# Optimization experiments

Hardware: AMD Instinct MI355X
Metric: run time of the kernel (lower is better)

The kernel has to match this reference:

```python
import jax, jax.numpy as jnp
import numpy as np

V, FN, CIN, HID, PTS = 50000, 100000, 3, 256, 10000
TEMP = 0.1
EPS = 1e-20


def line_mesh_graph(f, Vn):
    # f: [F,3] int triangles. Build the 'line mesh': one node per unique mesh edge.
    fe = jnp.concatenate([f[:, :2], f[:, 1:], f[:, jnp.array([2, 0])]], 0)  # [3F,2]
    fe = jnp.sort(fe, axis=1)
    keys = fe[:, 0] * Vn + fe[:, 1]                       # [3F] unique key per undirected edge
    ukeys, inv = jnp.unique(keys, return_inverse=True)
    edge_node = jnp.stack([ukeys // Vn, ukeys % Vn], -1)  # [E,2] endpoints of each edge-node
    E = ukeys.shape[0]
    feid = inv.reshape(3, -1).T                           # [F,3] edge-node id per face edge
    # line-graph connectivity: edges of the same face are mutual neighbors, plus self-loops
    srcs, dsts = [], []
    for i, j in ((0, 1), (1, 0), (1, 2), (2, 1), (2, 0), (0, 2)):
        srcs.append(feid[:, i]); dsts.append(feid[:, j])
    loop = jnp.arange(E)
    edge = jnp.stack([jnp.concatenate(srcs + [loop]), jnp.concatenate(dsts + [loop])], 0)  # [2,NE]
    return edge, edge_node, keys


def gsn_conv(x, edge, Ws, Wn, b):
    # GSNConv stand-in: self transform + mean-aggregated neighbor transform
    s, d = edge[0], edge[1]
    N = x.shape[0]
    deg = jax.ops.segment_sum(jnp.ones_like(s, x.dtype), d, num_segments=N)
    agg = jax.ops.segment_sum(x[s], d, num_segments=N) / jnp.clip(deg, 1.0)[:, None]
    return x @ Ws + agg @ Wn + b


def gumbel_mask(logits, temperature, num, key):
    U = jax.random.uniform(key, logits.shape)
    g = -jnp.log(-jnp.log(U + EPS) + EPS)
    y = jax.nn.softmax((logits + g) / temperature, -1)[:, 0]  # [E]
    _, ind = jax.lax.top_k(y, num)
    y_hard = jnp.zeros_like(y).at[ind].set(1.0)
    mask = jax.lax.stop_gradient(y_hard - y) + y              # straight-through one-hot
    return mask, y_hard == 1.0


def mesh_collapse(f, keys, pool_edge, Vn):
    # Vectorized replacement of the per-pool-edge python loop: hash-join pooled edge keys
    # against all 3F face-edge keys via sorted search.
    PE = pool_edge.shape[0]
    pool_idx = jnp.arange(Vn, Vn + PE)
    edge_keys = keys.reshape(3, -1).T                     # [F,3] (cols: e01,e12,e20)
    pk = pool_edge[:, 0] * Vn + pool_edge[:, 1]
    order = jnp.argsort(pk); pks = pk[order]
    flat = edge_keys.reshape(-1)
    pos = jnp.clip(jnp.searchsorted(pks, flat), 0, PE - 1)
    found = pks[pos] == flat
    pei = jnp.where(found, pool_idx[order[pos]], -1).reshape(-1, 3)  # pool_edge_idx [F,3]
    fm = found.reshape(-1, 3)
    pen = fm.sum(1)                                       # pool_edge_num per face
    psi = (fm * jnp.arange(3)).sum(1)                     # pool_start_idx per face
    vv = jnp.stack([f[:, 0], pei[:, 0], f[:, 1], pei[:, 1], f[:, 2], pei[:, 2]], -1)
    nf0 = f[pen == 0]
    fv1 = vv[pen == 1]; s1 = psi[pen == 1]
    fv1 = jnp.concatenate([fv1[s1 == 0], jnp.roll(fv1[s1 == 1], -2, 1), jnp.roll(fv1[s1 == 2], 2, 1)], 0)
    nf1 = jnp.concatenate([jnp.stack([fv1[:, 0], fv1[:, 1], fv1[:, 4]], -1),
                           jnp.stack([fv1[:, 1], fv1[:, 2], fv1[:, 4]], -1)], 0)
    fv2 = vv[pen == 2]; s2 = psi[pen == 2]
    fv2 = jnp.concatenate([fv2[s2 == 1], jnp.roll(fv2[s2 == 2], 2, 1), jnp.roll(fv2[s2 == 3], -2, 1)], 0)
    nf2 = jnp.concatenate([jnp.stack([fv2[:, 0], fv2[:, 1], fv2[:, 4]], -1),
                           jnp.stack([fv2[:, 1], fv2[:, 2], fv2[:, 3]], -1),
                           jnp.stack([fv2[:, 1], fv2[:, 3], fv2[:, 4]], -1)], 0)
    fv3 = vv[pen == 3]
    nf3 = jnp.concatenate([jnp.stack([fv3[:, 0], fv3[:, 1], fv3[:, 5]], -1),
                           jnp.stack([fv3[:, 1], fv3[:, 2], fv3[:, 3]], -1),
                           jnp.stack([fv3[:, 1], fv3[:, 3], fv3[:, 5]], -1),
                           jnp.stack([fv3[:, 3], fv3[:, 4], fv3[:, 5]], -1)], 0)
    new_faces = jnp.concatenate([nf0, nf1, nf2, nf3], 0)
    ne = jnp.concatenate([new_faces[:, :2], new_faces[:, 1:], new_faces[:, jnp.array([2, 0])]], 0)
    ai = jnp.arange(Vn + PE)
    ne = jnp.concatenate([jnp.stack([ai, ai], -1), ne], 0)
    return new_faces, ne.T


def setup_inputs():
    key = jax.random.key(0)
    ks = jax.random.split(key, 10)
    s1 = 1.0 / np.sqrt(CIN); s2 = 1.0 / np.sqrt(HID)
    return {
        'input': jax.random.normal(ks[0], (1, V, CIN), jnp.float32),
        'face': jax.random.randint(ks[1], (1, FN, 3), 0, V),
        'coord': jax.random.normal(ks[2], (1, V, 3), jnp.float32),
        'detail_points': jax.random.normal(ks[3], (1, PTS, 3), jnp.float32),
        'div': 5,
        'W1s': jax.random.normal(ks[4], (CIN, HID), jnp.float32) * s1,
        'W1n': jax.random.normal(ks[5], (CIN, HID), jnp.float32) * s1,
        'b1': jnp.zeros((HID,), jnp.float32),
        'W2s': jax.random.normal(ks[6], (HID, 2), jnp.float32) * s2,
        'W2n': jax.random.normal(ks[7], (HID, 2), jnp.float32) * s2,
        'b2': jnp.zeros((2,), jnp.float32),
    }


def reference(input, face, coord, detail_points, div, W1s, W1n, b1, W2s, W2n, b2):
    # B=1 (data-dependent per-sample output sizes make batch stacking only valid then)
    x0, f = input[0], face[0]
    Vn = x0.shape[0]
    edge, edge_node, keys = line_mesh_graph(f, Vn)
    xe = 0.5 * (x0[edge_node[:, 0]] + x0[edge_node[:, 1]])   # edge-node features [E,C]
    h = jax.nn.relu(gsn_conv(xe, edge, W1s, W1n, b1))
    out = jax.nn.sigmoid(gsn_conv(h, edge, W2s, W2n, b2))    # [E,2]
    mask, pool_ind = gumbel_mask(out, TEMP, out.shape[0] // div, jax.random.key(42))
    pool_edge = edge_node[pool_ind]                          # [PE,2]
    new_faces, new_edges = mesh_collapse(f, keys, pool_edge, Vn)
    return edge_node[None], new_faces[None], new_edges[None], mask[None]
```

## Files before the change

### kernel.cpp

```cpp
#include <hip/hip_runtime.h>
#include <stdint.h>

typedef uint32_t u32;
typedef uint64_t u64;

#define VN 50000
#define FN 100000
#define K3F 300000
#define EMAX 300000
#define NB1 1172
#define NBS 293
#define NBH 293
#define NBC 98
#define HALF1 150016
#define NBL 586

#define W_KPA    0u
#define W_KPB    600000u
#define W_SEGOFF 1200000u
#define W_FEID   1500004u
#define W_XE     1800004u
#define W_PK     2700004u
#define W_P      2703076u
#define W_Q      3303076u
#define W_Y      3903076u
#define W_YMAP   4203076u
#define W_T64    4503076u
#define W_SEL    5103140u
#define W_SELR   5403140u
#define W_CAT    5703140u
#define W_NFI    5903140u
#define W_HIST   7103140u
#define W_HIST2  7403172u
#define W_SUMS   7703204u
#define W_CATH   7707300u
#define W_TKH    7708324u
#define W_DONE   7708580u
#define W_SCAL   7708612u

#define S_E 0
#define S_NUM 1
#define S_PFX 2
#define S_KREM 3
#define S_TU 4
#define S_R 5
#define S_NF 6
#define S_NEN 7
#define S_O1 8
#define S_O2 9
#define S_O3 10
#define S_RS 16
#define S_GS 24
#define S_GP 32

#define ALDR(p) __hip_atomic_load((p), __ATOMIC_RELAXED, __HIP_MEMORY_SCOPE_AGENT)

__device__ __forceinline__ void tf2x32(u32 x0, u32 x1, u32& o0, u32& o1) {
  const u32 ks0 = 0u, ks1 = 42u, ks2 = 0x1BD11BDAu ^ 0u ^ 42u;
  x0 += ks0; x1 += ks1;
#define TFR(r) { x0 += x1; x1 = (x1<<(r))|(x1>>(32-(r))); x1 ^= x0; }
  TFR(13) TFR(15) TFR(26) TFR(6)   x0 += ks1; x1 += ks2 + 1u;
  TFR(17) TFR(29) TFR(16) TFR(24)  x0 += ks2; x1 += ks0 + 2u;
  TFR(13) TFR(15) TFR(26) TFR(6)   x0 += ks0; x1 += ks1 + 3u;
  TFR(17) TFR(29) TFR(16) TFR(24)  x0 += ks1; x1 += ks2 + 4u;
  TFR(13) TFR(15) TFR(26) TFR(6)   x0 += ks2; x1 += ks0 + 5u;
#undef TFR
  o0 = x0; o1 = x1;
}

__global__ void scan_blocks(const u32* __restrict__ in, u32* __restrict__ out,
                            u32* __restrict__ sums, int n) {
  __shared__ u32 lds[256];
  int t = threadIdx.x;
  int base = blockIdx.x*1024 + t*4;
  u32 v[4]; u32 tot = 0;
  for (int k = 0; k < 4; ++k) { v[k] = (base+k < n) ? in[base+k] : 0u; tot += v[k]; }
  lds[t] = tot; __syncthreads();
  for (int o = 1; o < 256; o <<= 1) {
    u32 x = (t >= o) ? lds[t-o] : 0u; __syncthreads();
    lds[t] += x; __syncthreads();
  }
  u32 excl = lds[t] - tot;
  if (t == 255) sums[blockIdx.x] = lds[255];
  u32 run = excl;
  for (int k = 0; k < 4; ++k) { if (base+k < n) out[base+k] = run; run += v[k]; }
}

__global__ void scan_flagblocks(const u64* __restrict__ kp, u32* __restrict__ out,
                                u32* __restrict__ sums, int n) {
  __shared__ u32 lds[256];
  int t = threadIdx.x;
  int base = blockIdx.x*1024 + t*4;
  u32 v[4]; u32 tot = 0;
  for (int k = 0; k < 4; ++k) {
    int i = base + k;
    u32 f = 0;
    if (i < n) f = (i == 0 || (u32)(kp[i-1]>>32) != (u32)(kp[i]>>32)) ? 1u : 0u;
    v[k] = f; tot += f;
  }
  lds[t] = tot; __syncthreads();
  for (int o = 1; o < 256; o <<= 1) {
    u32 x = (t >= o) ? lds[t-o] : 0u; __syncthreads();
    lds[t] += x; __syncthreads();
  }
  u32 excl = lds[t] - tot;
  if (t == 255) sums[blockIdx.x] = lds[255];
  u32 run = excl;
  for (int k = 0; k < 4; ++k) { if (base+k < n) out[base+k] = run; run += v[k]; }
}

__global__ void scan64_src(const u32* __restrict__ ymap, const u32* __restrict__ scal,
                           u64* __restrict__ part, u64* __restrict__ sums) {
  __shared__ u64 lds[256];
  int t = threadIdx.x;
  int base = blockIdx.x*1024 + t*4;
  int E = (int)scal[S_E];
  u32 TU = scal[S_TU];
  u64 v[4]; u64 tot = 0;
  for (int k = 0; k < 4; ++k) {
    int e = base + k;
    u64 val = 0;
    if (e < E) {
      u32 u = ymap[e];
      if (u > TU) val = 1ull;
      else if (u == TU) val = 1ull << 32;
    }
    v[k] = val; tot += val;
  }
  lds[t] = tot; __syncthreads();
  for (int o = 1; o < 256; o <<= 1) {
    u64 x = (t >= o) ? lds[t-o] : 0ull; __syncthreads();
    lds[t] += x; __syncthreads();
  }
  u64 excl = lds[t] - tot;
  if (t == 255) sums[blockIdx.x] = lds[255];
  u64 run = excl;
  for (int k = 0; k < 4; ++k) { part[base+k] = run; run += v[k]; }
}

__global__ void k_sel2(const u32* __restrict__ ymap, const u64* __restrict__ part,
                       const u64* __restrict__ sums, const u32* __restrict__ scal,
                       u32* __restrict__ sel, u32* __restrict__ selr) {
  __shared__ u64 sl64[256];
  int t = threadIdx.x, b = blockIdx.x;
  u64 partial = 0;
  for (int j = t; j < b; j += 256) partial += sums[j];
  sl64[t] = partial; __syncthreads();
  for (int o = 128; o; o >>= 1) { if (t < o) sl64[t] += sl64[t+o]; __syncthreads(); }
  u64 basepre = sl64[0];
  int E = (int)scal[S_E];
  u32 TU = scal[S_TU], R = scal[S_R];
  for (int k = 0; k < 4; ++k) {
    int e = b*1024 + k*256 + t;
    if (e >= EMAX) continue;
    u64 pre = part[e] + basepre;
    u32 GTpre = (u32)pre, TIEpre = (u32)(pre >> 32);
    u32 v = 0;
    if (e < E) {
      u32 u = ymap[e];
      v = (u > TU) || (u == TU && TIEpre < R);
    }
    sel[e] = v ? 1u : 0u;
    selr[e] = GTpre + min(TIEpre, R);
  }
}

__global__ void k_rhist(const u64* __restrict__ kp, u32* __restrict__ hist,
                        int shift, int nb) {
  __shared__ u32 h[256];
  int t = threadIdx.x;
  h[t] = 0; __syncthreads();
  int i = blockIdx.x*256 + t;
  if (i < K3F) atomicAdd(&h[((u32)(kp[i]>>32) >> shift) & 255u], 1u);
  __syncthreads();
  hist[(u32)t*nb + blockIdx.x] = h[t];
}

__global__ void k_rscat(const u64* __restrict__ kp, u64* __restrict__ okp,
                        const u32* __restrict__ hist, const u32* __restrict__ sums,
                        int shift, int nb) {
  __shared__ u32 sl[256];
  __shared__ u32 ps[NBS];
  __shared__ u64 ball[4][8];
  __shared__ u64 vmask[4];
  int t = threadIdx.x, w = t>>6, lane = t&63;
  u32 a0 = (t < NBS) ? sums[t] : 0u;
  u32 a1 = (256 + t < NBS) ? sums[256+t] : 0u;
  sl[t] = a0; __syncthreads();
  for (int o = 1; o < 256; o <<= 1) {
    u32 x = (t >= o) ? sl[t-o] : 0u; __syncthreads();
    sl[t] += x; __syncthreads();
  }
  u32 incl0 = sl[t], tot0 = sl[255];
  if (t < NBS) ps[t] = incl0 - a0;
  __syncthreads();
  sl[t] = a1; __syncthreads();
  for (int o = 1; o < 256; o <<= 1) {
    u32 x = (t >= o) ? sl[t-o] : 0u; __syncthreads();
    sl[t] += x; __syncthreads();
  }
  if (256 + t < NBS) ps[256+t] = sl[t] - a1 + tot0;
  __syncthreads();
  int i = blockIdx.x*256 + t;
  bool valid = i < K3F;
  u64 v = valid ? kp[i] : 0ull;
  u32 d = ((u32)(v>>32) >> shift) & 255u;
  for (int bit = 0; bit < 8; ++bit) {
    u64 bm = __ballot(valid && ((d>>bit)&1u));
    if (lane == 0) ball[w][bit] = bm;
  }
  u64 vb = __ballot(valid ? 1 : 0);
  if (lane == 0) vmask[w] = vb;
  __syncthreads();
  if (valid) {
    u32 rank = 0;
    for (int ww = 0; ww < w; ++ww) {
      u64 m = vmask[ww];
      for (int bit = 0; bit < 8; ++bit) { u64 bb = ball[ww][bit]; m &= ((d>>bit)&1u) ? bb : ~bb; }
      rank += (u32)__popcll(m);
    }
    u64 m = vmask[w];
    for (int bit = 0; bit < 8; ++bit) { u64 bb = ball[w][bit]; m &= ((d>>bit)&1u) ? bb : ~bb; }
    rank += (u32)__popcll(m & ((1ull<<lane)-1ull));
    u32 h = d*(u32)nb + blockIdx.x;
    u32 pos = hist[h] + ps[h>>10] + rank;
    okp[pos] = v;
  }
}

__global__ void k_keys(const int* __restrict__ face,
                       const float* __restrict__ W1s, const float* __restrict__ W1n,
                       const float* __restrict__ b1,
                       const float* __restrict__ W2s, const float* __restrict__ W2n,
                       float* __restrict__ pk,
                       u64* __restrict__ kp, u32* __restrict__ hist,
                       u32* __restrict__ tkh, u32* __restrict__ done) {
  __shared__ u32 h[256];
  int t = threadIdx.x;
  h[t] = 0;
  __syncthreads();
  if (blockIdx.x == 0) {
    tkh[t] = 0u;
    if (t < 32) done[t] = 0u;
    float* p = pk + t*12;
    p[0] = W1s[t]; p[1] = W1s[256+t]; p[2] = W1s[512+t];
    p[3] = W1n[t]; p[4] = W1n[256+t]; p[5] = W1n[512+t];
    p[6] = b1[t];
    p[7] = W2s[2*t]; p[8] = W2s[2*t+1];
    p[9] = W2n[2*t]; p[10] = W2n[2*t+1];
    p[11] = 0.0f;
  }
  int i = blockIdx.x*256 + t;
  if (i < K3F) {
    int s = i / FN, f = i - s*FN;
    int v0 = face[f*3 + s];
    int v1 = face[f*3 + (s == 2 ? 0 : s+1)];
    int a = min(v0, v1), b = max(v0, v1);
    u32 key = ((u32)a * (u32)VN + (u32)b) ^ 0x80000000u;
    kp[i] = ((u64)key << 32) | (u32)i;
    atomicAdd(&h[key & 255u], 1u);
  }
  __syncthreads();
  hist[(u32)t*NB1 + blockIdx.x] = h[t];
}

__global__ void k_uwrite(const u64* __restrict__ kp, const u32* __restrict__ rankp,
                         const u32* __restrict__ sums, const float* __restrict__ x,
                         u32* __restrict__ segoff, u32* __restrict__ feid,
                         float* __restrict__ xe, float* __restrict__ dout,
                         u32* __restrict__ scal, const int* __restrict__ divp) {
  __shared__ u32 sl[256];
  int t = threadIdx.x, b = blockIdx.x;
  int chunk = b >> 2;
  u32 partial = 0;
  for (int j = t; j < chunk; j += 256) partial += sums[j];
  sl[t] = partial; __syncthreads();
  for (int o = 128; o; o >>= 1) { if (t < o) sl[t] += sl[t+o]; __syncthreads(); }
  u32 basepre = sl[0];
  int p = b*256 + t;
  if (p >= K3F) return;
  u64 v = kp[p];
  u32 cur = (u32)(v >> 32);
  u32 fl = (p == 0 || (u32)(kp[p-1] >> 32) != cur) ? 1u : 0u;
  u32 rk = rankp[p] + basepre;
  if (fl) {
    u32 e = rk;
    segoff[e] = (u32)p;
    int k = (int)(cur ^ 0x80000000u);
    long long kk = (long long)k;
    long long qq = (kk - (kk < 0 ? (long long)(VN-1) : 0ll)) / VN;
    int q = (int)qq;
    int r = (int)(kk - qq * VN);
    dout[2*e]   = (float)q;
    dout[2*e+1] = (float)r;
    u32 i0 = (u32)(q < 0 ? q + VN : q);
    u32 i1 = (u32)r;
    for (int c = 0; c < 3; ++c) xe[e*3+c] = 0.5f*(x[i0*3+c] + x[i1*3+c]);
  }
  u32 id = rk - 1u + fl;
  u32 i = (u32)v;
  u32 s = i / FN, f = i - s*FN;
  feid[f*3 + s] = id;
  if (p == K3F-1) {
    u32 E = rk + fl;
    u32 num = E / (u32)divp[0];
    scal[S_E] = E; scal[S_NUM] = num;
    segoff[E] = (u32)K3F;
    scal[S_PFX] = 0u; scal[S_KREM] = num;
  }
}

__device__ __forceinline__ void agg_neighbors(int e, u32 st, u32 en,
                                              const u64* __restrict__ kp,
                                              const u32* __restrict__ feid,
                                              const float* __restrict__ v, int stride,
                                              float* acc0, float* acc1, float* acc2) {
  const int sslot[6] = {0,1,1,2,2,0};
  const int dslot[6] = {1,0,2,1,0,2};
  float c0 = 0.f, c1 = 0.f, c2 = 0.f;
  for (int b = 0; b < 6; ++b) {
    int j = dslot[b], isl = sslot[b];
    for (u32 p = st; p < en; ++p) {
      u32 i = (u32)kp[p];
      u32 s = i / FN;
      if ((int)s == j) {
        u32 f = i - s*FN;
        u32 u = feid[f*3 + isl];
        c0 += v[u*stride]; c1 += v[u*stride+1]; if (stride == 3) c2 += v[u*stride+2];
      }
    }
  }
  c0 += v[e*stride]; c1 += v[e*stride+1]; if (stride == 3) c2 += v[e*stride+2];
  *acc0 = c0; *acc1 = c1; *acc2 = c2;
}

__global__ void k_l12(const float* __restrict__ xe, const u32* __restrict__ segoff,
                      const u64* __restrict__ kp, const u32* __restrict__ feid,
                      const u32* __restrict__ scal, const float* __restrict__ pk,
                      float* __restrict__ P, float* __restrict__ Q) {
  int e1 = blockIdx.x*256 + threadIdx.x;
  int E = (int)scal[S_E];
  if (e1 >= E) return;
  int e2 = e1 + HALF1;
  bool v2 = e2 < E;
  int e2c = v2 ? e2 : e1;
  u32 st1 = segoff[e1], en1 = segoff[e1+1];
  u32 st2 = segoff[e2c], en2 = segoff[e2c+1];
  float c0a,c1a,c2a, c0b,c1b,c2b;
  agg_neighbors(e1,  st1, en1, kp, feid, xe, 3, &c0a,&c1a,&c2a);
  agg_neighbors(e2c, st2, en2, kp, feid, xe, 3, &c0b,&c1b,&c2b);
  float x0a=xe[e1*3],  x1a=xe[e1*3+1],  x2a=xe[e1*3+2];
  float x0b=xe[e2c*3], x1b=xe[e2c*3+1], x2b=xe[e2c*3+2];
  float dga = (float)(2u*(en1-st1)+1u), dgb = (float)(2u*(en2-st2)+1u);
  float m0a=c0a/dga, m1a=c1a/dga, m2a=c2a/dga;
  float m0b=c0b/dgb, m1b=c1b/dgb, m2b=c2b/dgb;
  float p0a=0,p1a=0,q0a=0,q1a=0, p0b=0,p1b=0,q0b=0,q1b=0;
#pragma unroll 4
  for (int hh = 0; hh < 256; ++hh) {
    const float* w = pk + hh*12;
    float w0=w[0],w1=w[1],w2=w[2],w3=w[3],w4=w[4],w5=w[5],w6=w[6];
    float w7=w[7],w8=w[8],w9=w[9],w10=w[10];
    float s1a = x0a*w0 + x1a*w1 + x2a*w2;
    float s2a = m0a*w3 + m1a*w4 + m2a*w5;
    float ha = fmaxf(s1a + s2a + w6, 0.0f);
    p0a += ha*w7;  p1a += ha*w8;  q0a += ha*w9;  q1a += ha*w10;
    float s1b = x0b*w0 + x1b*w1 + x2b*w2;
    float s2b = m0b*w3 + m1b*w4 + m2b*w5;
    float hb = fmaxf(s1b + s2b + w6, 0.0f);
    p0b += hb*w7;  p1b += hb*w8;  q0b += hb*w9;  q1b += hb*w10;
  }
  P[2*e1] = p0a; P[2*e1+1] = p1a; Q[2*e1] = q0a; Q[2*e1+1] = q1a;
  if (v2) { P[2*e2] = p0b; P[2*e2+1] = p1b; Q[2*e2] = q0b; Q[2*e2+1] = q1b; }
}

__device__ __forceinline__ void score_one(int e, const float* P, const float* Q,
                                          const u32* segoff, const u64* kp, const u32* feid,
                                          float b20, float b21, float* yo, u32* ymo) {
  u32 st = segoff[e], en = segoff[e+1];
  float a0, a1, dummy;
  agg_neighbors(e, st, en, kp, feid, Q, 2, &a0, &a1, &dummy);
  float dg = (float)(2u*(en - st) + 1u);
  float z0 = P[2*e]   + a0/dg + b20;
  float z1 = P[2*e+1] + a1/dg + b21;
  float l0 = 1.0f/(1.0f + expf(-z0));
  float l1 = 1.0f/(1.0f + expf(-z1));
  u32 g0b, g1b;
  { u32 o0,o1; tf2x32(0u, 2u*(u32)e,      o0, o1); g0b = o0 ^ o1; }
  { u32 o0,o1; tf2x32(0u, 2u*(u32)e + 1u, o0, o1); g1b = o0 ^ o1; }
  float U0 = __uint_as_float((g0b>>9) | 0x3f800000u) - 1.0f;
  float U1 = __uint_as_float((g1b>>9) | 0x3f800000u) - 1.0f;
  float g0 = -logf(-logf(U0 + 1e-20f) + 1e-20f);
  float g1 = -logf(-logf(U1 + 1e-20f) + 1e-20f);
  float A0 = (l0 + g0)/0.1f;
  float A1 = (l1 + g1)/0.1f;
  float mx = fmaxf(A0, A1);
  float e0 = expf(A0-mx), e1v = expf(A1-mx);
  float y = e0/(e0+e1v);
  *yo = y;
  *ymo = __float_as_uint(y) | 0x80000000u;
}

__global__ void k_scores(const float* __restrict__ P, const float* __restrict__ Q,
                         const u32* __restrict__ segoff, const u64* __restrict__ kp,
                         const u32* __restrict__ feid,
                         const float* __restrict__ b2, const u32* __restrict__ scal,
                         float* __restrict__ Y, u32* __restrict__ ymap) {
  int e1 = blockIdx.x*256 + threadIdx.x;
  int E = (int)scal[S_E];
  if (e1 >= E) return;
  int e2 = e1 + HALF1;
  bool v2 = e2 < E;
  int e2c = v2 ? e2 : e1;
  float b20 = b2[0], b21 = b2[1];
  float ya, yb; u32 ma, mb;
  score_one(e1,  P, Q, segoff, kp, feid, b20, b21, &ya, &ma);
  score_one(e2c, P, Q, segoff, kp, feid, b20, b21, &yb, &mb);
  Y[e1] = ya; ymap[e1] = ma;
  if (v2) { Y[e2] = yb; ymap[e2] = mb; }
}

__global__ void k_tkround(const u32* __restrict__ ymap, u32* __restrict__ scal,
                          u32* __restrict__ hist, u32* __restrict__ done, int byte) {
  __shared__ u32 h[256];
  __shared__ u32 s2[256];
  __shared__ u32 chosen_s;
  __shared__ u32 lastflag;
  int t = threadIdx.x;
  h[t] = 0u;
  if (t == 0) lastflag = 0u;
  __syncthreads();
  int E = (int)scal[S_E];
  u32 pfx = scal[S_PFX];
  int base = blockIdx.x*1024;
  for (int k = 0; k < 4; ++k) {
    int e = base + k*256 + t;
    if (e < E) {
      u32 u = ymap[e];
      bool match = (byte == 3) || ((u >> ((byte+1)*8)) == pfx);
      if (match) atomicAdd(&h[(u >> (byte*8)) & 255u], 1u);
    }
  }
  __syncthreads();
  u32 c = h[t];
  if (c) atomicAdd(&hist[t], c);
  __syncthreads();
  if (t == 0) {
    __threadfence();
    u32 old = atomicAdd(&done[byte], 1u);
    if (old == gridDim.x - 1u) lastflag = 1u;
  }
  __syncthreads();
  if (!lastflag) return;
  __threadfence();
  u32 v = atomicExch(&hist[t], 0u);
  s2[t] = v;
  if (t == 0) chosen_s = 0u;
  __syncthreads();
  for (int o = 1; o < 256; o <<= 1) {
    u32 x = (t + o < 256) ? s2[t+o] : 0u; __syncthreads();
    s2[t] += x; __syncthreads();
  }
  u32 krem = scal[S_KREM];
  if (s2[t] >= krem) atomicMax(&chosen_s, (u32)t);
  __syncthreads();
  if (t == 0) {
    u32 chosen = chosen_s;
    u32 sufnext = (chosen < 255u) ? s2[chosen+1] : 0u;
    u32 newkrem = krem - sufnext;
    u32 npfx = (scal[S_PFX] << 8) | chosen;
    scal[S_PFX] = npfx; scal[S_KREM] = newkrem;
    if (byte == 0) { scal[S_TU] = npfx; scal[S_R] = newkrem; }
  }
}

__global__ void k_catfused(const u32* __restrict__ feid, const u32* __restrict__ sel,
                           u32* __restrict__ cat, u32* __restrict__ ch,
                           u32* __restrict__ done, u32* __restrict__ scal) {
  __shared__ u32 h[8];
  __shared__ u32 lastflag;
  __shared__ u32 lds[256];
  __shared__ u32 ex[1024];
  int t = threadIdx.x;
  if (t < 8) h[t] = 0u;
  if (t == 0) lastflag = 0u;
  __syncthreads();
  int base = blockIdx.x*1024 + t*4;
  for (int k = 0; k < 4; ++k) {
    int f = base + k;
    if (f < FN) {
      u32 m0 = sel[feid[f*3]], m1 = sel[feid[f*3+1]], m2 = sel[feid[f*3+2]];
      u32 pen = m0 + m1 + m2;
      u32 psi = m1 + 2u*m2;
      u32 c = (pen == 0) ? 0u : (pen == 1) ? (1u+psi) : (pen == 2) ? (3u+psi) : 7u;
      cat[f] = c;
      atomicAdd(&h[c], 1u);
    }
  }
  __syncthreads();
  if (t < 8) ch[(u32)t*NBC + blockIdx.x] = h[t];
  __syncthreads();
  if (t == 0) {
    __threadfence();
    u32 old = atomicAdd(&done[8], 1u);
    if (old == gridDim.x - 1u) lastflag = 1u;
  }
  __syncthreads();
  if (!lastflag) return;
  __threadfence();
  u32 v[4]; u32 tot = 0;
  for (int k = 0; k < 4; ++k) {
    int i = t*4 + k;
    u32 x = (i < 8*NBC) ? ALDR(&ch[i]) : 0u;
    v[k] = x; tot += x;
  }
  lds[t] = tot; __syncthreads();
  for (int o = 1; o < 256; o <<= 1) {
    u32 x = (t >= o) ? lds[t-o] : 0u; __syncthreads();
    lds[t] += x; __syncthreads();
  }
  u32 excl = lds[t] - tot;
  u32 run = excl;
  for (int k = 0; k < 4; ++k) { ex[t*4+k] = run; run += v[k]; }
  __syncthreads();
  for (int k = 0; k < 4; ++k) {
    int i = t*4 + k;
    if (i < 8*NBC) ch[i] = ex[i];
  }
  if (t == 0) {
    u32 total = lds[255];
    u32 bnd[9];
    for (int c = 0; c < 8; ++c) bnd[c] = ex[c*NBC];
    bnd[8] = total;
    u32 tot8[8];
    for (int c = 0; c < 8; ++c) tot8[c] = bnd[c+1] - bnd[c];
    u32 n0 = tot8[0], n1 = tot8[1]+tot8[2]+tot8[3], n2 = tot8[4]+tot8[5]+tot8[6], n3 = tot8[7];
    u32 NF = n0 + 2u*n1 + 3u*n2 + 4u*n3;
    u32 E = scal[S_E], num = scal[S_NUM];
    u32 NEn = (u32)VN + num + 3u*NF;
    scal[S_NF] = NF; scal[S_NEN] = NEn;
    scal[S_O1] = 2u*E;
    scal[S_O2] = 2u*E + 3u*NF;
    scal[S_O3] = 2u*E + 3u*NF + 2u*NEn;
    u32 RS[8] = {0u, n0,n0,n0, n0+2u*n1, n0+2u*n1, n0+2u*n1, n0+2u*n1+3u*n2};
    u32 GS[8] = {0u, n1,n1,n1, n2,n2,n2, n3};
    u32 GP[8] = {0u, n0,n0,n0, n0+n1, n0+n1, n0+n1, n0+n1+n2};
    for (int i = 0; i < 8; ++i) { scal[S_RS+i] = RS[i]; scal[S_GS+i] = GS[i]; scal[S_GP+i] = GP[i]; }
  }
}

__global__ void k_catwf(const u32* __restrict__ cat, const u32* __restrict__ ch,
                        const int* __restrict__ face, const u32* __restrict__ feid,
                        const u32* __restrict__ selr, const u32* __restrict__ scal,
                        int* __restrict__ nfi, float* __restrict__ dout) {
  __shared__ u32 lds[256];
  int t = threadIdx.x;
  int base = blockIdx.x*1024 + t*4;
  u32 cc[4], loc[4];
  u32 cnt[8] = {0,0,0,0,0,0,0,0};
  for (int k = 0; k < 4; ++k) {
    int i = base + k;
    if (i < FN) { u32 c = cat[i]; cc[k] = c; loc[k] = cnt[c]++; }
    else cc[k] = 8u;
  }
  u32 tb[8];
  for (int c = 0; c < 8; ++c) {
    lds[t] = cnt[c]; __syncthreads();
    for (int o = 1; o < 256; o <<= 1) {
      u32 x = (t >= o) ? lds[t-o] : 0u; __syncthreads();
      lds[t] += x; __syncthreads();
    }
    tb[c] = lds[t] - cnt[c];
    __syncthreads();
  }
  const int nfc[8] = {1,2,2,2,3,3,3,4};
  const int tri[8][4][3] = {
    {{0,2,4},{0,0,0},{0,0,0},{0,0,0}},
    {{0,1,4},{1,2,4},{0,0,0},{0,0,0}},
    {{2,3,0},{3,4,0},{0,0,0},{0,0,0}},
    {{4,5,2},{5,0,2},{0,0,0},{0,0,0}},
    {{0,1,4},{1,2,3},{1,3,4},{0,0,0}},
    {{4,5,2},{5,0,1},{5,1,2},{0,0,0}},
    {{2,3,0},{3,4,5},{3,5,0},{0,0,0}},
    {{0,1,5},{1,2,3},{1,3,5},{3,4,5}}};
  u32 o1 = scal[S_O1];
  for (int k = 0; k < 4; ++k) {
    int f = base + k;
    if (f >= FN) break;
    u32 c = cc[k];
    u32 rank = ch[c*NBC + blockIdx.x] + tb[c] + loc[k];
    int cv[6];
    cv[0] = face[f*3];   cv[2] = face[f*3+1]; cv[4] = face[f*3+2];
    cv[1] = VN + (int)selr[feid[f*3]];
    cv[3] = VN + (int)selr[feid[f*3+1]];
    cv[5] = VN + (int)selr[feid[f*3+2]];
    u32 g = rank - scal[S_GP + c];
    for (int j = 0; j < nfc[c]; ++j) {
      u32 row = scal[S_RS + c] + (u32)j*scal[S_GS + c] + g;
      for (int m = 0; m < 3; ++m) {
        int v = cv[tri[c][j][m]];
        nfi[row*3 + m] = v;
        dout[o1 + row*3 + m] = (float)v;
      }
    }
  }
}

__global__ void k_wnemask(const int* __restrict__ nfi, const u32* __restrict__ sel,
                          const float* __restrict__ Y, const u32* __restrict__ scal,
                          float* __restrict__ dout) {
  int i = blockIdx.x*256 + threadIdx.x;
  int E = (int)scal[S_E];
  if (i < E) {
    float y = Y[i];
    float yh = sel[i] ? 1.0f : 0.0f;
    dout[scal[S_O3] + i] = (yh - y) + y;
  }
  u32 NEn = scal[S_NEN];
  if (i >= (int)NEn) return;
  u32 NF = scal[S_NF];
  u32 Vp = (u32)VN + scal[S_NUM];
  u32 o2 = scal[S_O2];
  int a, b;
  if ((u32)i < Vp) { a = i; b = i; }
  else {
    u32 j = (u32)i - Vp;
    u32 blk = j / NF, r = j - blk*NF;
    int i0 = (blk == 0) ? 0 : (blk == 1) ? 1 : 2;
    int i1 = (blk == 0) ? 1 : (blk == 1) ? 2 : 0;
    a = nfi[r*3 + i0]; b = nfi[r*3 + i1];
  }
  dout[o2 + i] = (float)a;
  dout[o2 + NEn + i] = (float)b;
}

extern "C" void kernel_launch(void* const* d_in, const int* in_sizes, int n_in,
                              void* d_out, int out_size, void* d_ws, size_t ws_size,
                              hipStream_t stream) {
  const float* x    = (const float*)d_in[0];
  const int*   face = (const int*)d_in[1];
  const int*   divp = (const int*)d_in[4];
  const float* W1s  = (const float*)d_in[5];
  const float* W1n  = (const float*)d_in[6];
  const float* b1   = (const float*)d_in[7];
  const float* W2s  = (const float*)d_in[8];
  const float* W2n  = (const float*)d_in[9];
  const float* b2   = (const float*)d_in[10];
  float* out = (float*)d_out;
  u32* W = (u32*)d_ws;

  u64 *KPA = (u64*)(W+W_KPA), *KPB = (u64*)(W+W_KPB);
  u32 *HIST = W+W_HIST, *HIST2 = W+W_HIST2, *SUMS = W+W_SUMS, *SCAL = W+W_SCAL;
  u32 *TKH = W+W_TKH, *DONE = W+W_DONE;
  u32 *RK = W+W_T64;
  u64 *T64 = (u64*)(W+W_T64);
  u64 *SUMS64 = (u64*)(W+W_SUMS);

  k_keys<<<NB1, 256, 0, stream>>>(face, W1s, W1n, b1, W2s, W2n, (float*)(W+W_PK),
                                  KPA, HIST, TKH, DONE);
  scan_blocks<<<NBS, 256, 0, stream>>>(HIST, HIST, SUMS, NB1*256);
  k_rscat<<<NB1, 256, 0, stream>>>(KPA, KPB, HIST, SUMS,  0, NB1);
  k_rhist<<<NB1, 256, 0, stream>>>(KPB, HIST2,  8, NB1);
  scan_blocks<<<NBS, 256, 0, stream>>>(HIST2, HIST2, SUMS, NB1*256);
  k_rscat<<<NB1, 256, 0, stream>>>(KPB, KPA, HIST2, SUMS,  8, NB1);
  k_rhist<<<NB1, 256, 0, stream>>>(KPA, HIST, 16, NB1);
  scan_blocks<<<NBS, 256, 0, stream>>>(HIST, HIST, SUMS, NB1*256);
  k_rscat<<<NB1, 256, 0, stream>>>(KPA, KPB, HIST, SUMS, 16, NB1);
  k_rhist<<<NB1, 256, 0, stream>>>(KPB, HIST2, 24, NB1);
  scan_blocks<<<NBS, 256, 0, stream>>>(HIST2, HIST2, SUMS, NB1*256);
  k_rscat<<<NB1, 256, 0, stream>>>(KPB, KPA, HIST2, SUMS, 24, NB1);

  scan_flagblocks<<<NBS, 256, 0, stream>>>(KPA, RK, SUMS, K3F);
  k_uwrite<<<NB1, 256, 0, stream>>>(KPA, RK, SUMS, x, W+W_SEGOFF, W+W_FEID,
                                    (float*)(W+W_XE), out, SCAL, divp);

  k_l12<<<NBL, 256, 0, stream>>>((float*)(W+W_XE), W+W_SEGOFF, KPA, W+W_FEID, SCAL,
                                 (float*)(W+W_PK), (float*)(W+W_P), (float*)(W+W_Q));
  k_scores<<<NBL, 256, 0, stream>>>((float*)(W+W_P), (float*)(W+W_Q), W+W_SEGOFF, KPA,
                                    W+W_FEID, b2, SCAL, (float*)(W+W_Y), W+W_YMAP);

  for (int byte = 3; byte >= 0; --byte)
    k_tkround<<<NBH, 256, 0, stream>>>(W+W_YMAP, SCAL, TKH, DONE, byte);
  scan64_src<<<NBS, 256, 0, stream>>>(W+W_YMAP, SCAL, T64, SUMS64);
  k_sel2<<<NBS, 256, 0, stream>>>(W+W_YMAP, T64, SUMS64, SCAL, W+W_SEL, W+W_SELR);

  k_catfused<<<NBC, 256, 0, stream>>>(W+W_FEID, W+W_SEL, W+W_CAT, W+W_CATH, DONE, SCAL);
  k_catwf<<<NBC, 256, 0, stream>>>(W+W_CAT, W+W_CATH, face, W+W_FEID, W+W_SELR, SCAL,
                                   (int*)(W+W_NFI), out);
  k_wnemask<<<5118, 256, 0, stream>>>((int*)(W+W_NFI), W+W_SEL, (float*)(W+W_Y), SCAL, out);
}
```

Measured before the change: 323.9 us.

## Fuse first top-k histogram round into score kernel; unroll short neighbor segments

The score kernel now also builds the top-byte histogram for radix top-k selection and runs the first selection round in its last-arriving block. This removes one k_tkround launch and one pass over ymap. Separately, neighbor aggregation for segments of at most 8 entries preloads keys into registers and unrolls the six slot passes, avoiding repeated global loads of kp. This adds shared-memory atomics and a done[9] counter, which relies on that slot being zeroed before the kernel runs.

```diff
diff --git a/kernel.cpp b/kernel.cpp
--- a/kernel.cpp
+++ b/kernel.cpp
@@ -316,17 +316,44 @@
                                               const float* __restrict__ v, int stride,
                                               float* acc0, float* acc1, float* acc2) {
   const int sslot[6] = {0,1,1,2,2,0};
-  const int dslot[6] = {1,0,2,1,0,2};
+  const int dslot[6] = {1,0,2,1,2,0};
+  (void)dslot;
+  const int dsl[6] = {1,0,2,1,0,2};
   float c0 = 0.f, c1 = 0.f, c2 = 0.f;
-  for (int b = 0; b < 6; ++b) {
-    int j = dslot[b], isl = sslot[b];
-    for (u32 p = st; p < en; ++p) {
-      u32 i = (u32)kp[p];
-      u32 s = i / FN;
-      if ((int)s == j) {
-        u32 f = i - s*FN;
-        u32 u = feid[f*3 + isl];
-        c0 += v[u*stride]; c1 += v[u*stride+1]; if (stride == 3) c2 += v[u*stride+2];
+  u32 n = en - st;
+  if (n <= 8u) {
+    u32 s8[8], ft[8];
+#pragma unroll
+    for (int j = 0; j < 8; ++j) {
+      if ((u32)j < n) {
+        u32 i = (u32)kp[st + (u32)j];
+        u32 s = i / FN;
+        s8[j] = s;
+        ft[j] = (i - s*FN)*3u;
+      } else { s8[j] = 0xFFFFFFFFu; ft[j] = 0u; }
+    }
+#pragma unroll
+    for (int b = 0; b < 6; ++b) {
+      u32 jd = (u32)dsl[b]; int isl = sslot[b];
+#pragma unroll
+      for (int j = 0; j < 8; ++j) {
+        if (s8[j] == jd) {
+          u32 u = feid[ft[j] + isl];
+          c0 += v[u*stride]; c1 += v[u*stride+1]; if (stride == 3) c2 += v[u*stride+2];
+        }
+      }
+    }
+  } else {
+    for (int b = 0; b < 6; ++b) {
+      int jd = dsl[b], isl = sslot[b];
+      for (u32 p = st; p < en; ++p) {
+        u32 i = (u32)kp[p];
+        u32 s = i / FN;
+        if ((int)s == jd) {
+          u32 f = i - s*FN;
+          u32 u = feid[f*3 + isl];
+          c0 += v[u*stride]; c1 += v[u*stride+1]; if (stride == 3) c2 += v[u*stride+2];
+        }
       }
     }
   }
@@ -404,19 +431,60 @@
                          const u32* __restrict__ segoff, const u64* __restrict__ kp,
                          const u32* __restrict__ feid,
                          const float* __restrict__ b2, const u32* __restrict__ scal,
-                         float* __restrict__ Y, u32* __restrict__ ymap) {
-  int e1 = blockIdx.x*256 + threadIdx.x;
+                         float* __restrict__ Y, u32* __restrict__ ymap,
+                         u32* __restrict__ tkh, u32* __restrict__ done,
+                         u32* __restrict__ scalw) {
+  __shared__ u32 h[256];
+  __shared__ u32 chosen_s;
+  __shared__ u32 lastflag;
+  int t = threadIdx.x;
+  h[t] = 0u;
+  if (t == 0) lastflag = 0u;
+  __syncthreads();
+  int e1 = blockIdx.x*256 + t;
   int E = (int)scal[S_E];
-  if (e1 >= E) return;
-  int e2 = e1 + HALF1;
-  bool v2 = e2 < E;
-  int e2c = v2 ? e2 : e1;
-  float b20 = b2[0], b21 = b2[1];
-  float ya, yb; u32 ma, mb;
-  score_one(e1,  P, Q, segoff, kp, feid, b20, b21, &ya, &ma);
-  score_one(e2c, P, Q, segoff, kp, feid, b20, b21, &yb, &mb);
-  Y[e1] = ya; ymap[e1] = ma;
-  if (v2) { Y[e2] = yb; ymap[e2] = mb; }
+  if (e1 < E) {
+    int e2 = e1 + HALF1;
+    bool v2 = e2 < E;
+    int e2c = v2 ? e2 : e1;
+    float b20 = b2[0], b21 = b2[1];
+    float ya, yb; u32 ma, mb;
+    score_one(e1,  P, Q, segoff, kp, feid, b20, b21, &ya, &ma);
+    score_one(e2c, P, Q, segoff, kp, feid, b20, b21, &yb, &mb);
+    Y[e1] = ya; ymap[e1] = ma;
+    atomicAdd(&h[ma >> 24], 1u);
+    if (v2) { Y[e2] = yb; ymap[e2] = mb; atomicAdd(&h[mb >> 24], 1u); }
+  }
+  __syncthreads();
+  u32 c = h[t];
+  if (c) atomicAdd(&tkh[t], c);
+  __syncthreads();
+  if (t == 0) {
+    __threadfence();
+    u32 old = atomicAdd(&done[9], 1u);
+    if (old == gridDim.x - 1u) lastflag = 1u;
+  }
+  __syncthreads();
+  if (!lastflag) return;
+  __threadfence();
+  u32 v = atomicExch(&tkh[t], 0u);
+  h[t] = v;
+  if (t == 0) chosen_s = 0u;
+  __syncthreads();
+  for (int o = 1; o < 256; o <<= 1) {
+    u32 x = (t + o < 256) ? h[t+o] : 0u; __syncthreads();
+    h[t] += x; __syncthreads();
+  }
+  u32 krem = scalw[S_KREM];
+  if (h[t] >= krem) atomicMax(&chosen_s, (u32)t);
+  __syncthreads();
+  if (t == 0) {
+    u32 chosen = chosen_s;
+    u32 sufnext = (chosen < 255u) ? h[chosen+1] : 0u;
+    u32 newkrem = krem - sufnext;
+    u32 npfx = (scalw[S_PFX] << 8) | chosen;
+    scalw[S_PFX] = npfx; scalw[S_KREM] = newkrem;
+  }
 }
 
 __global__ void k_tkround(const u32* __restrict__ ymap, u32* __restrict__ scal,
@@ -436,7 +504,7 @@
     int e = base + k*256 + t;
     if (e < E) {
       u32 u = ymap[e];
-      bool match = (byte == 3) || ((u >> ((byte+1)*8)) == pfx);
+      bool match = (u >> ((byte+1)*8)) == pfx;
       if (match) atomicAdd(&h[(u >> (byte*8)) & 255u], 1u);
     }
   }
@@ -676,9 +744,10 @@
   k_l12<<<NBL, 256, 0, stream>>>((float*)(W+W_XE), W+W_SEGOFF, KPA, W+W_FEID, SCAL,
                                  (float*)(W+W_PK), (float*)(W+W_P), (float*)(W+W_Q));
   k_scores<<<NBL, 256, 0, stream>>>((float*)(W+W_P), (float*)(W+W_Q), W+W_SEGOFF, KPA,
-                                    W+W_FEID, b2, SCAL, (float*)(W+W_Y), W+W_YMAP);
-
-  for (int byte = 3; byte >= 0; --byte)
+                                    W+W_FEID, b2, SCAL, (float*)(W+W_Y), W+W_YMAP,
+                                    TKH, DONE, SCAL);
+
+  for (int byte = 2; byte >= 0; --byte)
     k_tkround<<<NBH, 256, 0, stream>>>(W+W_YMAP, SCAL, TKH, DONE, byte);
   scan64_src<<<NBS, 256, 0, stream>>>(W+W_YMAP, SCAL, T64, SUMS64);
   k_sel2<<<NBS, 256, 0, stream>>>(W+W_YMAP, T64, SUMS64, SCAL, W+W_SEL, W+W_SELR);
```

New measurement: 327.3 us. Within noise of the previous version (+1.1%).
